# Kernel tuning notes

Measured on AMD Instinct MI355X. Metric: run time of the kernel, lower is better.

Reference implementation:

```python
import jax, jax.numpy as jnp
import numpy as np

B, S, HID = 1, 8192, 768
H, D = 12, 64          # num heads, head dim (HID = H*D)
W = 256                # one-sided attention window


def _shift_chunks(xc, C):
    # xc: [B, C, w, H, D] -> prev/next chunk copies padded with zeros
    prev = jnp.pad(xc, ((0, 0), (1, 0), (0, 0), (0, 0), (0, 0)))[:, :C]
    nxt = jnp.pad(xc, ((0, 0), (0, 1), (0, 0), (0, 0), (0, 0)))[:, 1:]
    return jnp.concatenate([prev, xc, nxt], axis=2)  # [B, C, 3w, H, D]


def sliding_window_attention(q, k, v, w):
    # q,k,v: [B, S, H, D]; q already scaled. Band width 2w+1.
    b, s, h, d = q.shape
    c = s // w
    qc = q.reshape(b, c, w, h, d)
    k3 = _shift_chunks(k.reshape(b, c, w, h, d), c)  # [b,c,3w,h,d]
    v3 = _shift_chunks(v.reshape(b, c, w, h, d), c)
    # scores of each query chunk against its 3-chunk key neighborhood
    scores3 = jnp.einsum('bcxhd,bcyhd->bhcxy', qc, k3)  # [b,h,c,w,3w]
    rows = jnp.arange(w)
    offs = jnp.arange(2 * w + 1)
    gidx = rows[:, None] + offs[None, :]  # [w, 2w+1] local key index p+j
    band = scores3[..., rows[:, None], gidx]  # [b,h,c,w,2w+1]
    # mask keys outside [0, S) (same effect as mask_invalid_locations)
    gq = jnp.arange(s).reshape(c, w)                    # global query pos
    keypos = gq[..., None] + (offs - w)                 # [c,w,2w+1]
    valid = (keypos >= 0) & (keypos < s)
    band = jnp.where(valid[None, None], band, -jnp.inf)
    prob = jax.nn.softmax(band, axis=-1)
    prob = jnp.where(valid[None, None], prob, 0.0)
    # scatter band probs back to 3w layout, then banded PV matmul
    prob3 = jnp.zeros(band.shape[:-1] + (3 * w,), band.dtype)
    prob3 = prob3.at[..., rows[:, None], gidx].set(prob)  # [b,h,c,w,3w]
    ctx = jnp.einsum('bhcxy,bcyhd->bcxhd', prob3, v3)
    return ctx.reshape(b, s, h, d)


def setup_inputs() -> dict:
    key = jax.random.key(0)
    ks = jax.random.split(key, 4)
    sc = 1.0 / np.sqrt(HID)
    return {
        'hidden_states': jax.random.normal(ks[0], (B, S, HID), jnp.float32),
        'Wq': jax.random.normal(ks[1], (HID, HID), jnp.float32) * sc,
        'bq': jnp.zeros((HID,), jnp.float32),
        'Wk': jax.random.normal(ks[2], (HID, HID), jnp.float32) * sc,
        'bk': jnp.zeros((HID,), jnp.float32),
        'Wv': jax.random.normal(ks[3], (HID, HID), jnp.float32) * sc,
        'bv': jnp.zeros((HID,), jnp.float32),
    }


def reference(hidden_states, Wq, bq, Wk, bk, Wv, bv):
    b, s, hid = hidden_states.shape
    q = (hidden_states @ Wq + bq).reshape(b, s, H, D)
    k = (hidden_states @ Wk + bk).reshape(b, s, H, D)
    v = (hidden_states @ Wv + bv).reshape(b, s, H, D)
    q = q / jnp.asarray(np.sqrt(D), q.dtype)
    ctx = sliding_window_attention(q, k, v, W)  # [b,s,H,D]
    return ctx.reshape(b, s, hid)
```

## Files before the change

### kernel.cpp

```cpp
#include <hip/hip_runtime.h>
#include <hip/hip_bf16.h>

#define S_LEN 8192
#define HID 768
#define NH 12
#define HD 64
#define WIN 256

typedef __bf16 bf16x8 __attribute__((ext_vector_type(8)));
typedef float f32x4 __attribute__((ext_vector_type(4)));
using bf16_t = __hip_bfloat16;

#define MFMA(a, b, c) __builtin_amdgcn_mfma_f32_16x16x32_bf16(a, b, c, 0, 0, 0)

__device__ __forceinline__ void gl2lds16(const bf16_t* g, bf16_t* l) {
  __builtin_amdgcn_global_load_lds(
      (const __attribute__((address_space(1))) void*)g,
      (__attribute__((address_space(3))) void*)l, 16, 0, 0);
}

__global__ __launch_bounds__(256) void prep(const float* __restrict__ hs,
                                            bf16_t* __restrict__ hb,
                                            const float* __restrict__ Wq,
                                            const float* __restrict__ Wk,
                                            const float* __restrict__ Wv,
                                            bf16_t* __restrict__ Wt) {
  int bx = blockIdx.x;
  int tid = threadIdx.x;
  if (bx < 6144) {
    int i = (bx * 256 + tid) * 4;
    float4 v = *reinterpret_cast<const float4*>(hs + i);
    union { ushort4 u; bf16_t b[4]; } H;
    H.b[0] = __float2bfloat16(v.x);
    H.b[1] = __float2bfloat16(v.y);
    H.b[2] = __float2bfloat16(v.z);
    H.b[3] = __float2bfloat16(v.w);
    *reinterpret_cast<ushort4*>(hb + i) = H.u;
    return;
  }
  __shared__ float t[32][33];
  int b = bx - 6144;
  int z = b / 576;
  int r = b % 576;
  int n0 = (r / 24) * 32, k0 = (r % 24) * 32;
  const float* src = (z == 0) ? Wq : ((z == 1) ? Wk : Wv);
  int tx = tid & 31, ty = tid >> 5;
  for (int i = 0; i < 4; ++i)
    t[ty + i * 8][tx] = src[(k0 + ty + i * 8) * HID + n0 + tx];
  __syncthreads();
  bf16_t* dst = Wt + z * HID * HID;
  for (int i = 0; i < 4; ++i)
    dst[(n0 + ty + i * 8) * HID + k0 + tx] = __float2bfloat16(t[tx][ty + i * 8]);
}

__global__ __launch_bounds__(256) void qkv_gemm(
    const bf16_t* __restrict__ hb, const bf16_t* __restrict__ Wt,
    const float* __restrict__ bq, const float* __restrict__ bk,
    const float* __restrict__ bv,
    bf16_t* __restrict__ Qw, bf16_t* __restrict__ Kw, bf16_t* __restrict__ Vt) {
  __shared__ __align__(16) bf16_t sA[2][128 * 64];
  __shared__ __align__(16) bf16_t sB[2][128 * 64];
  int bl = blockIdx.y * 64 + blockIdx.x;
  int xcd = bl & 7;
  int j = bl >> 3;
  int m0 = (xcd * 8 + (j & 7)) * 128;
  int rest = j >> 3;
  int zq = rest / 6;
  int nn0 = (rest % 6) * 128;
  int n0g = zq * HID + nn0;
  int tid = threadIdx.x;
  int w = tid >> 6, lane = tid & 63, lm = lane & 15, qd = lane >> 4;
  int wm = w & 1, wn = w >> 1;

  int srow = w * 8 + (lane >> 3);
  int sc8 = (lane & 7) ^ ((lane >> 3) & 7);
  const bf16_t* gA = hb + (m0 + srow) * HID + sc8 * 8;
  const bf16_t* gB = Wt + (n0g + srow) * HID + sc8 * 8;
  int sx0 = lm & 7;

#define QSTAGE(kk, bb)                                                     \
  {                                                                        \
    _Pragma("unroll") for (int u = 0; u < 4; ++u) {                        \
      gl2lds16(gA + (u * 32) * HID + (kk), sA[bb] + u * 2048 + w * 512);   \
      gl2lds16(gB + (u * 32) * HID + (kk), sB[bb] + u * 2048 + w * 512);   \
    }                                                                      \
  }

  QSTAGE(0, 0);
  __syncthreads();

  f32x4 acc[4][4] = {};
  for (int kt = 0; kt < 12; ++kt) {
    int b = kt & 1;
    if (kt < 11) QSTAGE((kt + 1) * 64, b ^ 1);
#pragma unroll
    for (int half = 0; half < 2; ++half) {
      int ca = (qd + 4 * half) ^ sx0;
      bf16x8 fa[4], fb[4];
#pragma unroll
      for (int i = 0; i < 4; ++i) {
        fa[i] = *reinterpret_cast<const bf16x8*>(
            sA[b] + (wm * 64 + i * 16 + lm) * 64 + ca * 8);
        fb[i] = *reinterpret_cast<const bf16x8*>(
            sB[b] + (wn * 64 + i * 16 + lm) * 64 + ca * 8);
      }
      if (zq == 2) {
#pragma unroll
        for (int i = 0; i < 4; ++i)
#pragma unroll
          for (int j2 = 0; j2 < 4; ++j2)
            acc[i][j2] = MFMA(fb[i], fa[j2], acc[i][j2]);
      } else {
#pragma unroll
        for (int i = 0; i < 4; ++i)
#pragma unroll
          for (int j2 = 0; j2 < 4; ++j2)
            acc[i][j2] = MFMA(fa[i], fb[j2], acc[i][j2]);
      }
    }
    __syncthreads();
  }

  if (zq != 2) {
    const float* bias = zq ? bk : bq;
    bf16_t* dst = zq ? Kw : Qw;
    float scale = zq ? 1.0f : 0.125f;
#pragma unroll
    for (int j2 = 0; j2 < 4; ++j2) {
      int nl = nn0 + wn * 64 + j2 * 16 + lm;
      float bb = bias[nl];
      int h = nl >> 6, d = nl & 63;
#pragma unroll
      for (int i = 0; i < 4; ++i)
#pragma unroll
        for (int r = 0; r < 4; ++r) {
          int m = m0 + wm * 64 + i * 16 + qd * 4 + r;
          dst[(h * S_LEN + m) * HD + d] =
              __float2bfloat16((acc[i][j2][r] + bb) * scale);
        }
    }
  } else {
#pragma unroll
    for (int i = 0; i < 4; ++i)
#pragma unroll
      for (int r = 0; r < 4; ++r) {
        int nl = nn0 + wn * 64 + i * 16 + qd * 4 + r;
        float bb = bv[nl];
#pragma unroll
        for (int j2 = 0; j2 < 4; ++j2) {
          int m = m0 + wm * 64 + j2 * 16 + lm;
          Vt[nl * S_LEN + m] = __float2bfloat16(acc[i][j2][r] + bb);
        }
      }
  }
}

__global__ __launch_bounds__(256, 3) void swa_kernel(
    const bf16_t* __restrict__ Qw, const bf16_t* __restrict__ Kw,
    const bf16_t* __restrict__ Vt, float* __restrict__ out) {
  __shared__ __align__(16) bf16_t sK[2][64 * 64];
  __shared__ __align__(16) bf16_t sV[2][64 * 64];
  __shared__ __align__(16) bf16_t sP[4 * 32 * 64];
  int h = blockIdx.y;
  int nb = blockIdx.x;
  int q0 = (((nb & 7) << 3) | (nb >> 3)) * 128;
  int tid = threadIdx.x;
  int w = tid >> 6, lane = tid & 63, lm = lane & 15, qd = lane >> 4;
  int xb = q0 + w * 32;

  int qoff = (h * S_LEN + xb + lm) * HD + qd * 8;
  bf16x8 aq00 = *reinterpret_cast<const bf16x8*>(Qw + qoff);
  bf16x8 aq01 = *reinterpret_cast<const bf16x8*>(Qw + qoff + 32);
  bf16x8 aq10 = *reinterpret_cast<const bf16x8*>(Qw + qoff + 16 * HD);
  bf16x8 aq11 = *reinterpret_cast<const bf16x8*>(Qw + qoff + 16 * HD + 32);

  f32x4 o0[4] = {}, o1[4] = {};
  float lsum0 = 0.f, lsum1 = 0.f;

  int y_begin = q0 - WIN; if (y_begin < 0) y_begin = 0;
  int y_end = q0 + 128 + WIN; if (y_end > S_LEN) y_end = S_LEN;
  int ntiles = (y_end - y_begin) >> 6;
  const bf16_t* Kh = Kw + h * S_LEN * HD;
  const bf16_t* Vh = Vt + h * HD * S_LEN;
  bf16_t* sPw = sP + w * 32 * 64;

  int srow = w * 8 + (lane >> 3);
  int sc8 = (lane & 7) ^ ((lane >> 3) & 7);
  int sx0 = lm & 7;

#define STAGE(y0, b)                                                    \
  {                                                                     \
    const bf16_t* kg = Kh + ((y0) + srow) * HD + sc8 * 8;               \
    gl2lds16(kg, &sK[b][w * 512]);                                      \
    gl2lds16(kg + 32 * HD, &sK[b][2048 + w * 512]);                     \
    const bf16_t* vg = Vh + srow * S_LEN + (y0) + sc8 * 8;              \
    gl2lds16(vg, &sV[b][w * 512]);                                      \
    gl2lds16(vg + 32 * S_LEN, &sV[b][2048 + w * 512]);                  \
  }

  STAGE(y_begin, 0);
  __syncthreads();

  for (int t = 0; t < ntiles; ++t) {
    int y0 = y_begin + t * 64;
    if (t + 1 < ntiles) STAGE(y0 + 64, (t + 1) & 1);
    int b = t & 1;
    f32x4 s0[4] = {}, s1[4] = {};
#pragma unroll
    for (int nt = 0; nt < 4; ++nt) {
      const bf16_t* kr = &sK[b][(nt * 16 + lm) * 64];
      bf16x8 b0 = *reinterpret_cast<const bf16x8*>(kr + (qd ^ sx0) * 8);
      bf16x8 b1 = *reinterpret_cast<const bf16x8*>(kr + ((qd + 4) ^ sx0) * 8);
      s0[nt] = MFMA(b0, aq00, s0[nt]);
      s0[nt] = MFMA(b1, aq01, s0[nt]);
      s1[nt] = MFMA(b0, aq10, s1[nt]);
      s1[nt] = MFMA(b1, aq11, s1[nt]);
    }
    int dyw = y0 - xb;
    bool edge = (dyw > 193) || (dyw < -225);
#pragma unroll
    for (int g = 0; g < 2; ++g) {
      const f32x4* sg = g ? s1 : s0;
      float lacc = 0.f;
#pragma unroll
      for (int nt = 0; nt < 4; ++nt) {
        union { ushort4 u; bf16_t b[4]; } P;
#pragma unroll
        for (int r = 0; r < 4; ++r) {
          float pv;
          if (edge) {
            int dlt = (y0 + nt * 16 + qd * 4 + r) - (xb + g * 16 + lm);
            pv = (dlt <= WIN && dlt >= -WIN) ? __expf(sg[nt][r]) : 0.f;
          } else {
            pv = __expf(sg[nt][r]);
          }
          lacc += pv;
          P.b[r] = __float2bfloat16(pv);
        }
        *reinterpret_cast<ushort4*>(
            sPw + (g * 16 + lm) * 64 +
            (((2 * nt + (qd >> 1)) ^ sx0) * 8) + (qd & 1) * 4) = P.u;
      }
      if (g) lsum1 += lacc; else lsum0 += lacc;
    }
    bf16x8 ap00 =
        *reinterpret_cast<const bf16x8*>(sPw + lm * 64 + ((qd ^ sx0) * 8));
    bf16x8 ap01 = *reinterpret_cast<const bf16x8*>(sPw + lm * 64 +
                                                   (((qd + 4) ^ sx0) * 8));
    bf16x8 ap10 = *reinterpret_cast<const bf16x8*>(sPw + (16 + lm) * 64 +
                                                   ((qd ^ sx0) * 8));
    bf16x8 ap11 = *reinterpret_cast<const bf16x8*>(sPw + (16 + lm) * 64 +
                                                   (((qd + 4) ^ sx0) * 8));
#pragma unroll
    for (int nt = 0; nt < 4; ++nt) {
      const bf16_t* vr = &sV[b][(nt * 16 + lm) * 64];
      bf16x8 v0 = *reinterpret_cast<const bf16x8*>(vr + (qd ^ sx0) * 8);
      bf16x8 v1 = *reinterpret_cast<const bf16x8*>(vr + ((qd + 4) ^ sx0) * 8);
      o0[nt] = MFMA(ap00, v0, o0[nt]);
      o0[nt] = MFMA(ap01, v1, o0[nt]);
      o1[nt] = MFMA(ap10, v0, o1[nt]);
      o1[nt] = MFMA(ap11, v1, o1[nt]);
    }
    __syncthreads();
  }
  lsum0 += __shfl_xor(lsum0, 16);
  lsum0 += __shfl_xor(lsum0, 32);
  lsum1 += __shfl_xor(lsum1, 16);
  lsum1 += __shfl_xor(lsum1, 32);
#pragma unroll
  for (int r = 0; r < 4; ++r) {
    float inv0 = 1.f / __shfl(lsum0, qd * 4 + r);
    int x0 = xb + qd * 4 + r;
#pragma unroll
    for (int nt = 0; nt < 4; ++nt)
      out[x0 * HID + h * HD + nt * 16 + lm] = o0[nt][r] * inv0;
    float inv1 = 1.f / __shfl(lsum1, qd * 4 + r);
    int x1 = xb + 16 + qd * 4 + r;
#pragma unroll
    for (int nt = 0; nt < 4; ++nt)
      out[x1 * HID + h * HD + nt * 16 + lm] = o1[nt][r] * inv1;
  }
}

extern "C" void kernel_launch(void* const* d_in, const int* in_sizes, int n_in,
                              void* d_out, int out_size, void* d_ws, size_t ws_size,
                              hipStream_t stream) {
  const float* hs = (const float*)d_in[0];
  const float* Wq = (const float*)d_in[1];
  const float* bq = (const float*)d_in[2];
  const float* Wk = (const float*)d_in[3];
  const float* bk = (const float*)d_in[4];
  const float* Wv = (const float*)d_in[5];
  const float* bv = (const float*)d_in[6];
  float* out = (float*)d_out;

  const int NSH = S_LEN * HID;
  const int NW = 3 * HID * HID;
  bf16_t* p = (bf16_t*)d_ws;
  bf16_t* hb = p; p += NSH;
  bf16_t* Wt = p; p += NW;
  bf16_t* Qw = p; p += NSH;
  bf16_t* Kw = p; p += NSH;
  bf16_t* Vt = p; p += NSH;

  prep<<<dim3(6144 + 1728), dim3(256), 0, stream>>>(hs, hb, Wq, Wk, Wv, Wt);
  qkv_gemm<<<dim3(64, 18), dim3(256), 0, stream>>>(
      hb, Wt, bq, bk, bv, Qw, Kw, Vt);
  swa_kernel<<<dim3(64, 12), dim3(256), 0, stream>>>(Qw, Kw, Vt, out);
}
```

Before: 157.9 us.

## Fuse fp32-to-bf16 hidden-state conversion into QKV GEMM A-tile loading

Drops the separate hidden-state conversion pass from the prep kernel. The QKV GEMM now loads fp32 activations straight into registers, converts them to bf16 and writes them swizzled into LDS after the MFMA loop, so the register prefetch overlaps with compute. This removes a 25MB fp32 read plus a 12.5MB bf16 write and round trip. In exchange, each GEMM block rereads fp32 A tiles across the 18 N-tiles, which doubles A traffic, and the register staging adds register pressure.

```diff
diff --git a/kernel.cpp b/kernel.cpp
--- a/kernel.cpp
+++ b/kernel.cpp
@@ -19,27 +19,13 @@
       (__attribute__((address_space(3))) void*)l, 16, 0, 0);
 }
 
-__global__ __launch_bounds__(256) void prep(const float* __restrict__ hs,
-                                            bf16_t* __restrict__ hb,
-                                            const float* __restrict__ Wq,
+__global__ __launch_bounds__(256) void prep(const float* __restrict__ Wq,
                                             const float* __restrict__ Wk,
                                             const float* __restrict__ Wv,
                                             bf16_t* __restrict__ Wt) {
-  int bx = blockIdx.x;
+  __shared__ float t[32][33];
+  int b = blockIdx.x;
   int tid = threadIdx.x;
-  if (bx < 6144) {
-    int i = (bx * 256 + tid) * 4;
-    float4 v = *reinterpret_cast<const float4*>(hs + i);
-    union { ushort4 u; bf16_t b[4]; } H;
-    H.b[0] = __float2bfloat16(v.x);
-    H.b[1] = __float2bfloat16(v.y);
-    H.b[2] = __float2bfloat16(v.z);
-    H.b[3] = __float2bfloat16(v.w);
-    *reinterpret_cast<ushort4*>(hb + i) = H.u;
-    return;
-  }
-  __shared__ float t[32][33];
-  int b = bx - 6144;
   int z = b / 576;
   int r = b % 576;
   int n0 = (r / 24) * 32, k0 = (r % 24) * 32;
@@ -54,7 +40,7 @@
 }
 
 __global__ __launch_bounds__(256) void qkv_gemm(
-    const bf16_t* __restrict__ hb, const bf16_t* __restrict__ Wt,
+    const float* __restrict__ hs, const bf16_t* __restrict__ Wt,
     const float* __restrict__ bq, const float* __restrict__ bk,
     const float* __restrict__ bv,
     bf16_t* __restrict__ Qw, bf16_t* __restrict__ Kw, bf16_t* __restrict__ Vt) {
@@ -74,25 +60,56 @@
 
   int srow = w * 8 + (lane >> 3);
   int sc8 = (lane & 7) ^ ((lane >> 3) & 7);
-  const bf16_t* gA = hb + (m0 + srow) * HID + sc8 * 8;
+  const float* gAf = hs + (size_t)(m0 + srow) * HID + (lane & 7) * 8;
   const bf16_t* gB = Wt + (n0g + srow) * HID + sc8 * 8;
   int sx0 = lm & 7;
-
-#define QSTAGE(kk, bb)                                                     \
-  {                                                                        \
-    _Pragma("unroll") for (int u = 0; u < 4; ++u) {                        \
-      gl2lds16(gA + (u * 32) * HID + (kk), sA[bb] + u * 2048 + w * 512);   \
-      gl2lds16(gB + (u * 32) * HID + (kk), sB[bb] + u * 2048 + w * 512);   \
-    }                                                                      \
-  }
-
-  QSTAGE(0, 0);
+  int awr = srow * 64 + sc8 * 8;
+
+  float4 ra[8];
+
+#define QK_LOADA(kk)                                                   \
+  {                                                                    \
+    _Pragma("unroll") for (int u = 0; u < 4; ++u) {                    \
+      const float* s = gAf + (u * 32) * HID + (kk);                    \
+      ra[2 * u] = *reinterpret_cast<const float4*>(s);                 \
+      ra[2 * u + 1] = *reinterpret_cast<const float4*>(s + 4);         \
+    }                                                                  \
+  }
+
+#define QK_CVTWR(bb)                                                   \
+  {                                                                    \
+    _Pragma("unroll") for (int u = 0; u < 4; ++u) {                    \
+      union { uint4 q; bf16_t b[8]; } T;                               \
+      T.b[0] = __float2bfloat16(ra[2 * u].x);                          \
+      T.b[1] = __float2bfloat16(ra[2 * u].y);                          \
+      T.b[2] = __float2bfloat16(ra[2 * u].z);                          \
+      T.b[3] = __float2bfloat16(ra[2 * u].w);                          \
+      T.b[4] = __float2bfloat16(ra[2 * u + 1].x);                      \
+      T.b[5] = __float2bfloat16(ra[2 * u + 1].y);                      \
+      T.b[6] = __float2bfloat16(ra[2 * u + 1].z);                      \
+      T.b[7] = __float2bfloat16(ra[2 * u + 1].w);                      \
+      *reinterpret_cast<uint4*>(sA[bb] + u * 2048 + awr) = T.q;        \
+    }                                                                  \
+  }
+
+#define QK_BSTG(kk, bb)                                                \
+  {                                                                    \
+    _Pragma("unroll") for (int u = 0; u < 4; ++u)                      \
+      gl2lds16(gB + (u * 32) * HID + (kk), sB[bb] + u * 2048 + w * 512); \
+  }
+
+  QK_LOADA(0);
+  QK_BSTG(0, 0);
+  QK_CVTWR(0);
   __syncthreads();
 
   f32x4 acc[4][4] = {};
   for (int kt = 0; kt < 12; ++kt) {
     int b = kt & 1;
-    if (kt < 11) QSTAGE((kt + 1) * 64, b ^ 1);
+    if (kt < 11) {
+      QK_LOADA((kt + 1) * 64);
+      QK_BSTG((kt + 1) * 64, b ^ 1);
+    }
 #pragma unroll
     for (int half = 0; half < 2; ++half) {
       int ca = (qd + 4 * half) ^ sx0;
@@ -118,6 +135,7 @@
             acc[i][j2] = MFMA(fa[i], fb[j2], acc[i][j2]);
       }
     }
+    if (kt < 11) QK_CVTWR(b ^ 1);
     __syncthreads();
   }
 
@@ -297,14 +315,13 @@
   const int NSH = S_LEN * HID;
   const int NW = 3 * HID * HID;
   bf16_t* p = (bf16_t*)d_ws;
-  bf16_t* hb = p; p += NSH;
   bf16_t* Wt = p; p += NW;
   bf16_t* Qw = p; p += NSH;
   bf16_t* Kw = p; p += NSH;
   bf16_t* Vt = p; p += NSH;
 
-  prep<<<dim3(6144 + 1728), dim3(256), 0, stream>>>(hs, hb, Wq, Wk, Wv, Wt);
+  prep<<<dim3(1728), dim3(256), 0, stream>>>(Wq, Wk, Wv, Wt);
   qkv_gemm<<<dim3(64, 18), dim3(256), 0, stream>>>(
-      hb, Wt, bq, bk, bv, Qw, Kw, Vt);
+      hs, Wt, bq, bk, bv, Qw, Kw, Vt);
   swa_kernel<<<dim3(64, 12), dim3(256), 0, stream>>>(Qw, Kw, Vt, out);
 }
```

Result: slower. 177.0 us (+12.1%).
